# Performance work log

Hardware: AMD Instinct MI355X
Metric: run time of the kernel (lower is better)

Reference implementation:

```python
import jax, jax.numpy as jnp
import numpy as np

B, V, C, H, W, D = 1, 3, 64, 96, 96, 48


def bilinear_sample(feat, gx, gy):
    """torch F.grid_sample(mode='bilinear', padding_mode='zeros', align_corners=True).
    feat: (B, C, H, W); gx, gy: (B, N) normalized coords in [-1, 1]. Returns (B, C, N)."""
    Bf, Cf, Hf, Wf = feat.shape
    x = (gx + 1.0) * 0.5 * (Wf - 1)
    y = (gy + 1.0) * 0.5 * (Hf - 1)
    x0 = jnp.floor(x)
    y0 = jnp.floor(y)
    wx1 = x - x0
    wy1 = y - y0
    wx0 = 1.0 - wx1
    wy0 = 1.0 - wy1
    flat = feat.reshape(Bf, Cf, Hf * Wf)

    def gather(xi, yi):
        valid = (xi >= 0) & (xi <= Wf - 1) & (yi >= 0) & (yi <= Hf - 1)
        xi_c = jnp.clip(xi, 0, Wf - 1).astype(jnp.int32)
        yi_c = jnp.clip(yi, 0, Hf - 1).astype(jnp.int32)
        idx = (yi_c * Wf + xi_c)[:, None, :]  # (B,1,N), broadcast over C
        return jnp.take_along_axis(flat, idx, axis=2) * valid[:, None, :]

    out = (gather(x0, y0) * (wx0 * wy0)[:, None]
           + gather(x0 + 1, y0) * (wx1 * wy0)[:, None]
           + gather(x0, y0 + 1) * (wx0 * wy1)[:, None]
           + gather(x0 + 1, y0 + 1) * (wx1 * wy1)[:, None])
    return out


def src_grid(proj_mat, depth_values, Hs, Ws):
    """homo_warp grid computation. proj_mat: (B,3,4); depth_values: (B,D).
    Returns normalized gx, gy each of shape (B, D*Hs*Ws)."""
    xs = jnp.arange(Ws, dtype=jnp.float32)
    ys = jnp.arange(Hs, dtype=jnp.float32)
    gx_, gy_ = jnp.meshgrid(xs, ys)  # (Hs, Ws) each
    ref = jnp.stack([gx_.ravel(), gy_.ravel(), jnp.ones(Hs * Ws, jnp.float32)], 0)  # (3, HW)
    R = proj_mat[:, :, :3]
    T = proj_mat[:, :, 3]
    # (B,3,D,HW): R @ p + T / depth
    pts = jnp.einsum('bij,jn->bin', R, ref)[:, :, None, :] + T[:, :, None, None] / depth_values[:, None, :, None]
    xy = pts[:, :2] / pts[:, 2:3]
    gx = xy[:, 0] / ((Ws - 1) / 2.0) - 1.0
    gy = xy[:, 1] / ((Hs - 1) / 2.0) - 1.0
    Bb = proj_mat.shape[0]
    return gx.reshape(Bb, -1), gy.reshape(Bb, -1)


def setup_inputs() -> dict:
    key = jax.random.key(0)
    k1, k2, k3, k4 = jax.random.split(key, 4)
    imgs = jax.random.normal(k1, (B, V, 3, H, W), jnp.float32)
    feats = jax.random.normal(k2, (B, V, C, H, W), jnp.float32)
    # near-identity projections so warped coords land mostly in-range (z ~ 1)
    eye = jnp.broadcast_to(jnp.eye(3, dtype=jnp.float32), (B, V, 3, 3))
    Rn = eye + 0.05 * jax.random.normal(k3, (B, V, 3, 3), jnp.float32)
    Tn = 0.5 * jax.random.normal(jax.random.fold_in(k3, 1), (B, V, 3, 1), jnp.float32)
    proj_mats = jnp.concatenate([Rn, Tn], axis=-1)
    depth_values = 2.0 + 4.0 * jax.random.uniform(k4, (B, D), jnp.float32)
    return {"imgs": imgs, "feats": feats, "proj_mats": proj_mats, "depth_values": depth_values}


def reference(imgs, feats, proj_mats, depth_values):
    Bb, Vv, _, Hh, Ww = imgs.shape
    Cc = feats.shape[2]
    Dd = depth_values.shape[1]
    # ref view volume (broadcast over D)
    ref_volume = jnp.broadcast_to(feats[:, 0][:, :, None], (Bb, Cc, Dd, Hh, Ww))
    volume_sum = ref_volume
    volume_sq_sum = ref_volume ** 2
    mask_sum = jnp.ones((Bb, Dd, Hh, Ww), jnp.float32)  # ref view always in-range
    img_chans = [jnp.broadcast_to(imgs[:, 0][:, :, None], (Bb, 3, Dd, Hh, Ww))]
    for i in range(Vv - 1):  # small fixed number of source views
        gx, gy = src_grid(proj_mats[:, i + 1], depth_values, Hh, Ww)
        wv = bilinear_sample(feats[:, i + 1], gx, gy).reshape(Bb, Cc, Dd, Hh, Ww)
        wi = bilinear_sample(imgs[:, i + 1], gx, gy).reshape(Bb, 3, Dd, Hh, Ww)
        m = ((gx > -1.0) & (gx < 1.0) & (gy > -1.0) & (gy < 1.0)).astype(jnp.float32).reshape(Bb, Dd, Hh, Ww)
        volume_sum = volume_sum + wv
        volume_sq_sum = volume_sq_sum + wv ** 2
        mask_sum = mask_sum + m
        img_chans.append(wi)
    count = 1.0 / mask_sum[:, None]  # (B,1,D,H,W)
    var = volume_sq_sum * count - (volume_sum * count) ** 2  # (B,C,D,H,W)
    img_chans.append(var)
    return jnp.concatenate(img_chans, axis=1)  # (B, 3*V + C, D, H, W)
```

## Files before the change

kernel.cpp:

```cpp
#include <hip/hip_runtime.h>

#define BDIM 256

constexpr int Vv = 3, Cc = 64, Hh = 96, Ww = 96, Dd = 48;
constexpr int HW = Hh * Ww;
constexpr int NPIX = Dd * HW;
constexpr int DHW = Dd * HW;

__device__ __forceinline__ void compute_warp(const float* __restrict__ proj, float depth,
                                             float xf, float yf,
                                             int offs[2][4], float wts[2][4], float& msum)
{
    msum = 1.0f;
#pragma unroll
    for (int v = 0; v < 2; ++v) {
#pragma clang fp contract(off)
        const float* P = proj + (v + 1) * 12;
        const float r00 = P[0], r01 = P[1], r02 = P[2],  t0 = P[3];
        const float r10 = P[4], r11 = P[5], r12 = P[6],  t1 = P[7];
        const float r20 = P[8], r21 = P[9], r22 = P[10], t2 = P[11];

        const float px = ((r00 * xf + r01 * yf) + r02) + t0 / depth;
        const float py = ((r10 * xf + r11 * yf) + r12) + t1 / depth;
        const float pz = ((r20 * xf + r21 * yf) + r22) + t2 / depth;

        const float xy0 = px / pz;
        const float xy1 = py / pz;
        const float gx = xy0 / ((float)(Ww - 1) * 0.5f) - 1.0f;
        const float gy = xy1 / ((float)(Hh - 1) * 0.5f) - 1.0f;

        const bool inb = (gx > -1.0f) && (gx < 1.0f) && (gy > -1.0f) && (gy < 1.0f);
        msum += inb ? 1.0f : 0.0f;

        const float sx = (gx + 1.0f) * 0.5f * (float)(Ww - 1);
        const float sy = (gy + 1.0f) * 0.5f * (float)(Hh - 1);
        const float x0 = floorf(sx), y0 = floorf(sy);
        const float wx1 = sx - x0, wy1 = sy - y0;
        const float wx0 = 1.0f - wx1, wy0 = 1.0f - wy1;

#pragma unroll
        for (int k = 0; k < 4; ++k) {
            const float xi = (k & 1) ? (x0 + 1.0f) : x0;
            const float yi = (k & 2) ? (y0 + 1.0f) : y0;
            const float wk = ((k & 1) ? wx1 : wx0) * ((k & 2) ? wy1 : wy0);
            const bool valid = (xi >= 0.0f) && (xi <= (float)(Ww - 1)) &&
                               (yi >= 0.0f) && (yi <= (float)(Hh - 1));
            const float xc = fminf(fmaxf(xi, 0.0f), (float)(Ww - 1));
            const float yc = fminf(fmaxf(yi, 0.0f), (float)(Hh - 1));
            offs[v][k] = (int)yc * Ww + (int)xc;
            wts[v][k] = valid ? wk : 0.0f;
        }
    }
}

__global__ void __launch_bounds__(BDIM) transpose_feats_kernel(const float* __restrict__ feats,
                                                               float* __restrict__ ft)
{
    __shared__ float tile[64][65];
    const int v  = blockIdx.y;
    const int p0 = blockIdx.x * 64;
    const float* src = feats + (size_t)v * Cc * HW;

    const int px = threadIdx.x & 63;
    const int c0 = threadIdx.x >> 6;
#pragma unroll
    for (int c = c0; c < Cc; c += 4)
        tile[c][px] = src[(size_t)c * HW + p0 + px];
    __syncthreads();

    const int cc  = threadIdx.x & 63;
    const int pr0 = threadIdx.x >> 6;
    float* dst = ft + ((size_t)v * HW + p0) * Cc;
#pragma unroll
    for (int p = pr0; p < 64; p += 4)
        dst[p * Cc + cc] = tile[cc][p];
}

__global__ void __launch_bounds__(BDIM) ge_row_kernel(
    const float* __restrict__ imgs, const float* __restrict__ ftr,
    const float* __restrict__ proj, const float* __restrict__ depthv,
    float* __restrict__ out)
{
    __shared__ float s_tile[Cc][Ww + 1];
    __shared__ int   s_base[2][4][Ww];
    __shared__ float s_wt[2][4][Ww];
    __shared__ float s_cnt[Ww];

    const int blk = blockIdx.x;
    const int d   = blk / Hh;
    const int h   = blk % Hh;
    const int tid = threadIdx.x;
    const int rowbase = d * HW + h * Ww;

    if (tid < Ww) {
        const int w = tid;
        int offs[2][4];
        float wts[2][4];
        float msum;
        compute_warp(proj, depthv[d], (float)w, (float)h, offs, wts, msum);
        s_cnt[w] = 1.0f / msum;
#pragma unroll
        for (int v = 0; v < 2; ++v)
#pragma unroll
            for (int k = 0; k < 4; ++k) {
                s_base[v][k][w] = ((v + 1) * HW + offs[v][k]) * Cc;
                s_wt[v][k][w]   = wts[v][k];
            }

        const int hw = h * Ww + w;
#pragma unroll
        for (int c = 0; c < 3; ++c)
            out[c * DHW + rowbase + w] = imgs[c * HW + hw];

#pragma unroll
        for (int v = 0; v < 2; ++v) {
            const float* ib = imgs + (size_t)(v + 1) * 3 * HW;
#pragma unroll
            for (int c = 0; c < 3; ++c) {
                const float* p = ib + (size_t)c * HW;
                const float acc = wts[v][0] * p[offs[v][0]] + wts[v][1] * p[offs[v][1]] +
                                  wts[v][2] * p[offs[v][2]] + wts[v][3] * p[offs[v][3]];
                out[(3 * (v + 1) + c) * DHW + rowbase + w] = acc;
            }
        }
    }
    __syncthreads();

    {
        const int wave = tid >> 6;
        const int c    = tid & 63;
        const int p0   = wave * (Ww / 4);
#pragma unroll 2
        for (int i = 0; i < Ww / 4; ++i) {
            const int p = p0 + i;
            const float cnt = s_cnt[p];
            const int b00 = s_base[0][0][p], b01 = s_base[0][1][p];
            const int b02 = s_base[0][2][p], b03 = s_base[0][3][p];
            const int b10 = s_base[1][0][p], b11 = s_base[1][1][p];
            const int b12 = s_base[1][2][p], b13 = s_base[1][3][p];
            const float w00 = s_wt[0][0][p], w01 = s_wt[0][1][p];
            const float w02 = s_wt[0][2][p], w03 = s_wt[0][3][p];
            const float w10 = s_wt[1][0][p], w11 = s_wt[1][1][p];
            const float w12 = s_wt[1][2][p], w13 = s_wt[1][3][p];

            const float fr = ftr[(size_t)(h * Ww + p) * Cc + c];
            const float a1 = w00 * ftr[b00 + c] + w01 * ftr[b01 + c] +
                             w02 * ftr[b02 + c] + w03 * ftr[b03 + c];
            const float a2 = w10 * ftr[b10 + c] + w11 * ftr[b11 + c] +
                             w12 * ftr[b12 + c] + w13 * ftr[b13 + c];
            const float s  = fr + a1 + a2;
            const float q  = fr * fr + a1 * a1 + a2 * a2;
            const float sc = s * cnt;
            s_tile[c][p] = q * cnt - sc * sc;
        }
    }
    __syncthreads();

#pragma unroll
    for (int idx = tid; idx < Cc * Ww; idx += BDIM) {
        const int cc = idx / Ww;
        const int p  = idx - cc * Ww;
        out[(9 + cc) * DHW + rowbase + p] = s_tile[cc][p];
    }
}

__global__ void __launch_bounds__(BDIM) ge_direct_kernel(
    const float* __restrict__ imgs, const float* __restrict__ feats,
    const float* __restrict__ proj, const float* __restrict__ depthv,
    float* __restrict__ out)
{
    const int idx = blockIdx.x * BDIM + threadIdx.x;
    if (idx >= NPIX) return;
    const int w = idx % Ww;
    const int t = idx / Ww;
    const int h = t % Hh;
    const int d = t / Hh;
    const int ohw = h * Ww + w;

    int offs[2][4];
    float wts[2][4];
    float msum;
    compute_warp(proj, depthv[d], (float)w, (float)h, offs, wts, msum);

    const int obase = d * HW + ohw;
#pragma unroll
    for (int c = 0; c < 3; ++c)
        out[c * DHW + obase] = imgs[c * HW + ohw];

#pragma unroll
    for (int v = 0; v < 2; ++v) {
        const float* ib = imgs + (size_t)(v + 1) * 3 * HW;
#pragma unroll
        for (int c = 0; c < 3; ++c) {
            const float* p = ib + (size_t)c * HW;
            const float acc = wts[v][0] * p[offs[v][0]] + wts[v][1] * p[offs[v][1]] +
                              wts[v][2] * p[offs[v][2]] + wts[v][3] * p[offs[v][3]];
            out[(3 * (v + 1) + c) * DHW + obase] = acc;
        }
    }

    const float count = 1.0f / msum;
    const float* f0 = feats;
    const float* f1 = feats + (size_t)Cc * HW;
    const float* f2 = feats + (size_t)2 * Cc * HW;
#pragma unroll 8
    for (int c = 0; c < Cc; ++c) {
        const float fr = f0[(size_t)c * HW + ohw];
        const float* p1 = f1 + (size_t)c * HW;
        const float* p2 = f2 + (size_t)c * HW;
        const float a1 = wts[0][0] * p1[offs[0][0]] + wts[0][1] * p1[offs[0][1]] +
                         wts[0][2] * p1[offs[0][2]] + wts[0][3] * p1[offs[0][3]];
        const float a2 = wts[1][0] * p2[offs[1][0]] + wts[1][1] * p2[offs[1][1]] +
                         wts[1][2] * p2[offs[1][2]] + wts[1][3] * p2[offs[1][3]];
        const float s = fr + a1 + a2;
        const float sq = fr * fr + a1 * a1 + a2 * a2;
        const float sc = s * count;
        out[(3 * Vv + c) * DHW + obase] = sq * count - sc * sc;
    }
}

extern "C" void kernel_launch(void* const* d_in, const int* in_sizes, int n_in,
                              void* d_out, int out_size, void* d_ws, size_t ws_size,
                              hipStream_t stream)
{
    const float* imgs   = (const float*)d_in[0];
    const float* feats  = (const float*)d_in[1];
    const float* proj   = (const float*)d_in[2];
    const float* depthv = (const float*)d_in[3];
    float* out = (float*)d_out;

    const size_t need = (size_t)Vv * HW * Cc * sizeof(float);

    if (ws_size >= need) {
        float* ftr = (float*)d_ws;
        dim3 g1(HW / 64, Vv);
        transpose_feats_kernel<<<g1, BDIM, 0, stream>>>(feats, ftr);
        ge_row_kernel<<<Dd * Hh, BDIM, 0, stream>>>(imgs, ftr, proj, depthv, out);
    } else {
        const int blocks = (NPIX + BDIM - 1) / BDIM;
        ge_direct_kernel<<<blocks, BDIM, 0, stream>>>(imgs, feats, proj, depthv, out);
    }
}
```

Before: 180.6 us.

## Vectorize gather with float4 channels, pack base/weight pairs, nontemporal stores

Each lane of the row kernel now handles four consecutive channels with float4 loads from the transposed feature buffer, so 16 lanes cover one pixel instead of one lane per channel. Base offsets and weights are packed into float2 shared entries to halve the shared reads. The tile is padded to a stride of 100 with rotated column writes to limit bank conflicts, and the output is written back as 16-byte nontemporal stores. Loads and stores of streaming data use nontemporal hints to avoid polluting cache, though the rotated shared writes may still cause some conflicts.

```diff
diff --git a/kernel.cpp b/kernel.cpp
--- a/kernel.cpp
+++ b/kernel.cpp
@@ -6,6 +6,9 @@
 constexpr int HW = Hh * Ww;
 constexpr int NPIX = Dd * HW;
 constexpr int DHW = Dd * HW;
+constexpr int TSTR = 100;
+
+typedef float f32x4 __attribute__((ext_vector_type(4)));
 
 __device__ __forceinline__ void compute_warp(const float* __restrict__ proj, float depth,
                                              float xf, float yf,
@@ -65,7 +68,7 @@
     const int c0 = threadIdx.x >> 6;
 #pragma unroll
     for (int c = c0; c < Cc; c += 4)
-        tile[c][px] = src[(size_t)c * HW + p0 + px];
+        tile[c][px] = __builtin_nontemporal_load(&src[(size_t)c * HW + p0 + px]);
     __syncthreads();
 
     const int cc  = threadIdx.x & 63;
@@ -81,10 +84,9 @@
     const float* __restrict__ proj, const float* __restrict__ depthv,
     float* __restrict__ out)
 {
-    __shared__ float s_tile[Cc][Ww + 1];
-    __shared__ int   s_base[2][4][Ww];
-    __shared__ float s_wt[2][4][Ww];
-    __shared__ float s_cnt[Ww];
+    __shared__ float  s_tile[Cc][TSTR];
+    __shared__ float2 s_bw[2][4][Ww];
+    __shared__ float  s_cnt[Ww];
 
     const int blk = blockIdx.x;
     const int d   = blk / Hh;
@@ -103,14 +105,14 @@
         for (int v = 0; v < 2; ++v)
 #pragma unroll
             for (int k = 0; k < 4; ++k) {
-                s_base[v][k][w] = ((v + 1) * HW + offs[v][k]) * Cc;
-                s_wt[v][k][w]   = wts[v][k];
+                const int base = ((v + 1) * HW + offs[v][k]) * Cc;
+                s_bw[v][k][w] = make_float2(__int_as_float(base), wts[v][k]);
             }
 
         const int hw = h * Ww + w;
 #pragma unroll
         for (int c = 0; c < 3; ++c)
-            out[c * DHW + rowbase + w] = imgs[c * HW + hw];
+            __builtin_nontemporal_store(imgs[c * HW + hw], &out[c * DHW + rowbase + w]);
 
 #pragma unroll
         for (int v = 0; v < 2; ++v) {
@@ -120,7 +122,7 @@
                 const float* p = ib + (size_t)c * HW;
                 const float acc = wts[v][0] * p[offs[v][0]] + wts[v][1] * p[offs[v][1]] +
                                   wts[v][2] * p[offs[v][2]] + wts[v][3] * p[offs[v][3]];
-                out[(3 * (v + 1) + c) * DHW + rowbase + w] = acc;
+                __builtin_nontemporal_store(acc, &out[(3 * (v + 1) + c) * DHW + rowbase + w]);
             }
         }
     }
@@ -128,39 +130,66 @@
 
     {
         const int wave = tid >> 6;
-        const int c    = tid & 63;
-        const int p0   = wave * (Ww / 4);
+        const int lane = tid & 63;
+        const int sub  = lane >> 4;
+        const int cq   = lane & 15;
+        const int c4   = 4 * cq;
+        const float* ftr0 = ftr + (size_t)(h * Ww) * Cc;
+
 #pragma unroll 2
-        for (int i = 0; i < Ww / 4; ++i) {
-            const int p = p0 + i;
+        for (int g = 0; g < 6; ++g) {
+            const int p = wave * 24 + g * 4 + sub;
             const float cnt = s_cnt[p];
-            const int b00 = s_base[0][0][p], b01 = s_base[0][1][p];
-            const int b02 = s_base[0][2][p], b03 = s_base[0][3][p];
-            const int b10 = s_base[1][0][p], b11 = s_base[1][1][p];
-            const int b12 = s_base[1][2][p], b13 = s_base[1][3][p];
-            const float w00 = s_wt[0][0][p], w01 = s_wt[0][1][p];
-            const float w02 = s_wt[0][2][p], w03 = s_wt[0][3][p];
-            const float w10 = s_wt[1][0][p], w11 = s_wt[1][1][p];
-            const float w12 = s_wt[1][2][p], w13 = s_wt[1][3][p];
-
-            const float fr = ftr[(size_t)(h * Ww + p) * Cc + c];
-            const float a1 = w00 * ftr[b00 + c] + w01 * ftr[b01 + c] +
-                             w02 * ftr[b02 + c] + w03 * ftr[b03 + c];
-            const float a2 = w10 * ftr[b10 + c] + w11 * ftr[b11 + c] +
-                             w12 * ftr[b12 + c] + w13 * ftr[b13 + c];
-            const float s  = fr + a1 + a2;
-            const float q  = fr * fr + a1 * a1 + a2 * a2;
-            const float sc = s * cnt;
-            s_tile[c][p] = q * cnt - sc * sc;
+            const float2 bw00 = s_bw[0][0][p], bw01 = s_bw[0][1][p];
+            const float2 bw02 = s_bw[0][2][p], bw03 = s_bw[0][3][p];
+            const float2 bw10 = s_bw[1][0][p], bw11 = s_bw[1][1][p];
+            const float2 bw12 = s_bw[1][2][p], bw13 = s_bw[1][3][p];
+
+            const float4 fr  = *(const float4*)(ftr0 + (size_t)p * Cc + c4);
+            const float4 v00 = *(const float4*)(ftr + (size_t)__float_as_int(bw00.x) + c4);
+            const float4 v01 = *(const float4*)(ftr + (size_t)__float_as_int(bw01.x) + c4);
+            const float4 v02 = *(const float4*)(ftr + (size_t)__float_as_int(bw02.x) + c4);
+            const float4 v03 = *(const float4*)(ftr + (size_t)__float_as_int(bw03.x) + c4);
+            const float4 v10 = *(const float4*)(ftr + (size_t)__float_as_int(bw10.x) + c4);
+            const float4 v11 = *(const float4*)(ftr + (size_t)__float_as_int(bw11.x) + c4);
+            const float4 v12 = *(const float4*)(ftr + (size_t)__float_as_int(bw12.x) + c4);
+            const float4 v13 = *(const float4*)(ftr + (size_t)__float_as_int(bw13.x) + c4);
+
+            const float w00 = bw00.y, w01 = bw01.y, w02 = bw02.y, w03 = bw03.y;
+            const float w10 = bw10.y, w11 = bw11.y, w12 = bw12.y, w13 = bw13.y;
+
+            float var_[4];
+#define VARC(comp, j)                                                            \
+            {                                                                    \
+                const float A_ = w00 * v00.comp + w01 * v01.comp +               \
+                                 w02 * v02.comp + w03 * v03.comp;                \
+                const float B_ = w10 * v10.comp + w11 * v11.comp +               \
+                                 w12 * v12.comp + w13 * v13.comp;                \
+                const float F_ = fr.comp;                                        \
+                const float S_ = F_ + A_ + B_;                                   \
+                const float Q_ = F_ * F_ + A_ * A_ + B_ * B_;                    \
+                const float sc_ = S_ * cnt;                                      \
+                var_[j] = Q_ * cnt - sc_ * sc_;                                  \
+            }
+            VARC(x, 0) VARC(y, 1) VARC(z, 2) VARC(w, 3)
+#undef VARC
+#pragma unroll
+            for (int jj = 0; jj < 4; ++jj) {
+                const int col = (jj + cq) & 3;
+                s_tile[c4 + col][p] = var_[col];
+            }
         }
     }
     __syncthreads();
 
 #pragma unroll
-    for (int idx = tid; idx < Cc * Ww; idx += BDIM) {
-        const int cc = idx / Ww;
-        const int p  = idx - cc * Ww;
-        out[(9 + cc) * DHW + rowbase + p] = s_tile[cc][p];
+    for (int i = 0; i < 6; ++i) {
+        const int idx = i * BDIM + tid;
+        const int c   = idx / 24;
+        const int pp  = idx - c * 24;
+        const f32x4 vv = *(const f32x4*)&s_tile[c][pp * 4];
+        f32x4* dst = (f32x4*)(out + (size_t)(9 + c) * DHW + rowbase + pp * 4);
+        __builtin_nontemporal_store(vv, dst);
     }
 }
 
```

Result: no change. 182.7 us (+1.1%).
